# Kernel optimization log

Hardware: AMD Instinct MI355X
Metric: run time of the kernel (lower is better)

The kernel has to match this reference:

```python
import jax, jax.numpy as jnp
import numpy as np

NUM_EXPERTS = 64
TOP_K = 2
CAPACITY_FACTOR = 1.25
D_MODEL = 2048
BATCH, SEQ = 4, 4096


def setup_inputs() -> dict:
    key = jax.random.key(0)
    kx, kw = jax.random.split(key)
    x = jax.random.normal(kx, (BATCH, SEQ, D_MODEL), dtype=jnp.float32)
    # router weight: Linear(input_dim, num_experts, bias=False), init std=0.001
    W = jax.random.normal(kw, (NUM_EXPERTS, D_MODEL), dtype=jnp.float32) * 0.001
    return {"x": x, "W": W}


def reference(x, W):
    B, S, D = x.shape
    N = B * S  # combined batch of tokens
    E = NUM_EXPERTS
    k = TOP_K
    capacity = int(CAPACITY_FACTOR * N * k / E)  # static Python int

    x_flat = x.reshape(N, D)
    router_logits = jnp.einsum('nd,ed->ne', x_flat, W)  # [N, E]
    routing_weights = jax.nn.softmax(router_logits, axis=-1)

    top_k_weights, top_k_indices = jax.lax.top_k(routing_weights, k)  # [N, k]
    top_k_weights = top_k_weights / (top_k_weights.sum(-1, keepdims=True) + 1e-8)

    expert_counts = jnp.zeros((E,), dtype=jnp.float32)
    dispatch_mask = jnp.zeros((N, E), dtype=jnp.float32)
    token_ids = jnp.arange(N)

    # Sequential over k (fixed, small): within a k-step the capacity check uses
    # counts from previous steps only, matching the torch scatter semantics.
    for k_idx in range(k):
        expert_idx = top_k_indices[:, k_idx]            # [N]
        under_cap = expert_counts[expert_idx] < capacity  # [N] bool
        expert_counts = expert_counts + jax.ops.segment_sum(
            under_cap.astype(jnp.float32), expert_idx, num_segments=E)
        # top-k experts are distinct per token, so add == set on zero-init slots
        dispatch_mask = dispatch_mask.at[token_ids, expert_idx].add(
            jnp.where(under_cap, top_k_weights[:, k_idx], 0.0))

    # Tokens that got dropped everywhere go to the least-loaded expert with w=1
    unrouted = dispatch_mask.sum(-1) == 0                     # [N]
    least_loaded = jnp.argmax(capacity - expert_counts)       # scalar
    dispatch_mask = jnp.where(
        unrouted[:, None] & (jnp.arange(E)[None, :] == least_loaded),
        1.0, dispatch_mask)

    normalized_dispatch_mask = dispatch_mask / (dispatch_mask.sum(-1, keepdims=True) + 1e-8)

    router_z_loss = jnp.mean(jnp.square(router_logits))
    counts = normalized_dispatch_mask.sum(0)                  # [E]
    target_count = float(N * k / E)
    load_balance_loss = jnp.mean(jnp.square(counts / float(N) - target_count / float(N)))
    router_loss = 0.001 * jax.lax.stop_gradient(router_z_loss) \
                + 0.001 * jax.lax.stop_gradient(load_balance_loss)

    return (jax.lax.stop_gradient(routing_weights), normalized_dispatch_mask, router_loss)
```

## Files before the change

### kernel.cpp

```cpp
#include <hip/hip_runtime.h>
#include <math.h>

#define N_TOK 16384
#define D_MODEL 2048
#define N_EXP 64
#define CAPACITY 640
#define NREP 8
#define TM 32
#define NSTEP 32

typedef __attribute__((ext_vector_type(8))) _Float16 h8;
typedef __attribute__((ext_vector_type(4))) float f4;

#define AS1 __attribute__((address_space(1)))
#define AS3 __attribute__((address_space(3)))
__device__ __forceinline__ void gld16(const void* g, void* l) {
  __builtin_amdgcn_global_load_lds((const AS1 void*)g, (AS3 void*)l, 16, 0, 0);
}

__global__ __launch_bounds__(256) void k0_cvtw(const float* __restrict__ W,
                                               _Float16* __restrict__ WT) {
  const int lane = threadIdx.x & 63;
  const int c = blockIdx.x * 4 + (threadIdx.x >> 6);
  const int s = c >> 4, q = c & 15;
  const int part = q >> 3, ks = (q >> 2) & 1, nt = q & 3;
  const int e = nt * 16 + (lane & 15);
  const int k = s * 64 + ks * 32 + (lane >> 4) * 8;
  const float* src = W + (size_t)e * D_MODEL + k;
  const float4 a = *(const float4*)src;
  const float4 b = *(const float4*)(src + 4);
  const float f[8] = {a.x, a.y, a.z, a.w, b.x, b.y, b.z, b.w};
  h8 out;
#pragma unroll
  for (int j = 0; j < 8; j++) {
    const float sc = f[j] * 1024.f;
    const _Float16 h = (_Float16)sc;
    out[j] = part ? (_Float16)((sc - (float)h) * 1024.f) : h;
  }
  *(h8*)(WT + (size_t)c * 512 + lane * 8) = out;
}

__global__ __launch_bounds__(256, 2) void k12_gemm_softmax(
    const float* __restrict__ x, const _Float16* __restrict__ WT,
    float* __restrict__ rw_out, int2* __restrict__ top12,
    float2* __restrict__ wts, int* __restrict__ histR,
    float* __restrict__ zR) {
  __shared__ __align__(16) float XS[2][2048];
  __shared__ __align__(16) _Float16 WS[2][8192];
  __shared__ float slog[TM][65];
  __shared__ float zred[4];

  const int t = threadIdx.x;
  const int lane = t & 63;
  const int wid = t >> 6;
  const int m0 = blockIdx.x * TM;
  const int rep = blockIdx.x & (NREP - 1);

  const int i0 = wid * 2;
  const int r0 = i0 * 4 + (lane >> 4);
  const int r1 = r0 + 4;
  const int s16 = lane & 15;
  const float* xs0 = x + (size_t)(m0 + r0) * D_MODEL + ((s16 ^ (r0 & 7)) * 4);
  const float* xs1 = x + (size_t)(m0 + r1) * D_MODEL + ((s16 ^ (r1 & 7)) * 4);
  const _Float16* wsrc = WT + (size_t)(wid * 4) * 512 + lane * 8;

  f4 acc1[2], acc2[2];
#pragma unroll
  for (int i = 0; i < 2; i++) {
    acc1[i] = (f4)(0.f);
    acc2[i] = (f4)(0.f);
  }

#define STAGE(buf, s)                                           \
  {                                                             \
    gld16(xs0 + (s) * 64, &XS[buf][i0 * 256]);                  \
    gld16(xs1 + (s) * 64, &XS[buf][i0 * 256 + 256]);            \
    _Pragma("unroll") for (int j2 = 0; j2 < 4; j2++)            \
        gld16(wsrc + (size_t)(s) * 8192 + j2 * 512,             \
              &WS[buf][(wid * 4 + j2) * 512]);                  \
  }

#define COMPUTE(buf)                                                           \
  {                                                                            \
    _Pragma("unroll") for (int ks = 0; ks < 2; ks++) {                         \
      const h8 bh = *(const h8*)&WS[buf][(ks * 4 + wid) * 512 + lane * 8];     \
      const h8 bl = *(const h8*)&WS[buf][(8 + ks * 4 + wid) * 512 + lane * 8]; \
      _Pragma("unroll") for (int mf = 0; mf < 2; mf++) {                       \
        const int row = mf * 16 + (lane & 15);                                 \
        const int cb = ks * 8 + (lane >> 4) * 2;                               \
        const int sw = lane & 7;                                               \
        const f4 a0 = *(const f4*)&XS[buf][row * 64 + ((cb ^ sw) * 4)];        \
        const f4 a1 = *(const f4*)&XS[buf][row * 64 + (((cb + 1) ^ sw) * 4)];  \
        h8 ah, al;                                                             \
        const float xf[8] = {a0[0], a0[1], a0[2], a0[3],                       \
                             a1[0], a1[1], a1[2], a1[3]};                      \
        _Pragma("unroll") for (int j = 0; j < 8; j++) {                        \
          const _Float16 hv = (_Float16)xf[j];                                 \
          ah[j] = hv;                                                          \
          al[j] = (_Float16)((xf[j] - (float)hv) * 1024.f);                    \
        }                                                                      \
        acc1[mf] = __builtin_amdgcn_mfma_f32_16x16x32_f16(ah, bh, acc1[mf],    \
                                                          0, 0, 0);            \
        acc2[mf] = __builtin_amdgcn_mfma_f32_16x16x32_f16(al, bh, acc2[mf],    \
                                                          0, 0, 0);            \
        acc2[mf] = __builtin_amdgcn_mfma_f32_16x16x32_f16(ah, bl, acc2[mf],    \
                                                          0, 0, 0);            \
      }                                                                        \
    }                                                                          \
  }

  STAGE(0, 0);
  int cur = 0;
  for (int s = 0; s < NSTEP; s++) {
    __syncthreads();
    if (s + 1 < NSTEP) STAGE(cur ^ 1, s + 1);
    COMPUTE(cur);
    cur ^= 1;
  }

  const int cg = lane >> 4, ci = lane & 15;
#pragma unroll
  for (int mf = 0; mf < 2; mf++)
#pragma unroll
    for (int r = 0; r < 4; r++) {
      const float v =
          (acc1[mf][r] + acc2[mf][r] * 0.0009765625f) * 0.0009765625f;
      slog[mf * 16 + cg * 4 + r][wid * 16 + ci] = v;
    }
  __syncthreads();

  float z_acc = 0.f;
  for (int tt = 0; tt < 8; tt++) {
    const int tloc = wid * 8 + tt;
    const int n = m0 + tloc;
    const float v = slog[tloc][lane];
    z_acc += v * v;
    float mx = v;
#pragma unroll
    for (int off = 32; off; off >>= 1) mx = fmaxf(mx, __shfl_xor(mx, off));
    const float p = __expf(v - mx);
    float ssum = p;
#pragma unroll
    for (int off = 32; off; off >>= 1) ssum += __shfl_xor(ssum, off);
    const float rw = p / ssum;
    rw_out[(size_t)n * N_EXP + lane] = rw;

    const unsigned long long b1 = __ballot(v == mx);
    const int i1 = __builtin_ctzll(b1);
    float v2 = (lane == i1) ? -INFINITY : v;
#pragma unroll
    for (int off = 32; off; off >>= 1) v2 = fmaxf(v2, __shfl_xor(v2, off));
    const unsigned long long b2 = __ballot(v == v2) & ~(1ull << i1);
    const int i2 = __builtin_ctzll(b2);
    const float rw1 = __shfl(rw, i1);
    const float rw2 = __shfl(rw, i2);
    if (lane == 0) {
      const float denom = rw1 + rw2 + 1e-8f;
      top12[n] = make_int2(i1, i2);
      wts[n] = make_float2(rw1 / denom, rw2 / denom);
      atomicAdd(&histR[(rep * N_EXP + i1) * 16], 1);
    }
  }
#pragma unroll
  for (int off = 32; off; off >>= 1) z_acc += __shfl_xor(z_acc, off);
  if (lane == 0) zred[wid] = z_acc;
  __syncthreads();
  if (t == 0) atomicAdd(&zR[rep * 16], zred[0] + zred[1] + zred[2] + zred[3]);
}

__global__ __launch_bounds__(256) void k3_dispatch(
    const int2* __restrict__ top12, const float2* __restrict__ wts,
    const int* __restrict__ histR, float* __restrict__ mask_out,
    float* __restrict__ cntR) {
  const int lane = threadIdx.x & 63;
  const int wid = threadIdx.x >> 6;
  const int n = blockIdx.x * 4 + wid;
  const int rep = blockIdx.x & (NREP - 1);

  const int2 ij = top12[n];
  const float2 w = wts[n];
  int h = 0;
#pragma unroll
  for (int r = 0; r < NREP; r++) h += histR[(r * N_EXP + ij.y) * 16];
  const bool allowed = h < CAPACITY;
  const float ssum = w.x + (allowed ? w.y : 0.f);
  const float inv = 1.f / (ssum + 1e-8f);
  float val = 0.f;
  if (lane == ij.x) val = w.x * inv;
  else if (allowed && lane == ij.y) val = w.y * inv;
  mask_out[(size_t)n * N_EXP + lane] = val;
  if (val != 0.f) atomicAdd(&cntR[(rep * N_EXP + lane) * 16], val);
}

__global__ void k4_loss(const float* __restrict__ cntR,
                        const float* __restrict__ zR,
                        float* __restrict__ loss_out) {
  const int lane = threadIdx.x;
  float c = 0.f;
#pragma unroll
  for (int r = 0; r < NREP; r++) c += cntR[(r * N_EXP + lane) * 16];
  const float d = (c - 512.0f) * (1.0f / 16384.0f);
  float v = d * d;
#pragma unroll
  for (int off = 32; off; off >>= 1) v += __shfl_xor(v, off);
  if (lane == 0) {
    float z = 0.f;
#pragma unroll
    for (int r = 0; r < NREP; r++) z += zR[r * 16];
    const float lb = v * (1.0f / 64.0f);
    loss_out[0] = 0.001f * (z * (1.0f / (16384.0f * 64.0f))) + 0.001f * lb;
  }
}

extern "C" void kernel_launch(void* const* d_in, const int* in_sizes, int n_in,
                              void* d_out, int out_size, void* d_ws,
                              size_t ws_size, hipStream_t stream) {
  const float* x = (const float*)d_in[0];
  const float* W = (const float*)d_in[1];
  float* out = (float*)d_out;
  float* rw_out = out;
  float* mask_out = out + (size_t)N_TOK * N_EXP;
  float* loss_out = out + 2 * (size_t)N_TOK * N_EXP;

  char* ws = (char*)d_ws;
  int* histR = (int*)ws;
  float* cntR = (float*)(ws + 32768);
  float* zR = (float*)(ws + 65536);
  int2* top12 = (int2*)(ws + 131072);
  float2* wts = (float2*)(ws + 262144);
  _Float16* WT = (_Float16*)(ws + 393216);

  hipMemsetAsync(histR, 0, 65536 + 512, stream);
  k0_cvtw<<<128, 256, 0, stream>>>(W, WT);
  k12_gemm_softmax<<<512, 256, 0, stream>>>(x, WT, rw_out, top12, wts, histR,
                                            zR);
  k3_dispatch<<<N_TOK / 4, 256, 0, stream>>>(top12, wts, histR, mask_out,
                                             cntR);
  k4_loss<<<1, 64, 0, stream>>>(cntR, zR, loss_out);
}
```

Baseline: 228.9 us.

## Make GEMM warps independent with per-warp triple-buffered LDS pipeline

Restructures the router GEMM so each of two waves owns a 16-token tile across all 64 experts, with its own triple-buffered LDS staging driven by vmcnt waits instead of block-wide barriers. This removes __syncthreads from the k-loop and the cross-wave softmax handoff, and regroups the W fp16 split layout into k-steps of 32. The cost is that every wave now loads the full W slice on its own, so W traffic per token doubles, and blocks shrink to 128 threads.

Result: slower. 234.8 us (+2.6%).

```diff
diff --git a/kernel.cpp b/kernel.cpp
--- a/kernel.cpp
+++ b/kernel.cpp
@@ -6,8 +6,7 @@
 #define N_EXP 64
 #define CAPACITY 640
 #define NREP 8
-#define TM 32
-#define NSTEP 32
+#define NSTEP 64
 
 typedef __attribute__((ext_vector_type(8))) _Float16 h8;
 typedef __attribute__((ext_vector_type(4))) float f4;
@@ -22,10 +21,10 @@
                                                _Float16* __restrict__ WT) {
   const int lane = threadIdx.x & 63;
   const int c = blockIdx.x * 4 + (threadIdx.x >> 6);
-  const int s = c >> 4, q = c & 15;
-  const int part = q >> 3, ks = (q >> 2) & 1, nt = q & 3;
+  const int s = c >> 3, q = c & 7;
+  const int part = q >> 2, nt = q & 3;
   const int e = nt * 16 + (lane & 15);
-  const int k = s * 64 + ks * 32 + (lane >> 4) * 8;
+  const int k = s * 32 + (lane >> 4) * 8;
   const float* src = W + (size_t)e * D_MODEL + k;
   const float4 a = *(const float4*)src;
   const float4 b = *(const float4*)(src + 4);
@@ -40,100 +39,96 @@
   *(h8*)(WT + (size_t)c * 512 + lane * 8) = out;
 }
 
-__global__ __launch_bounds__(256, 2) void k12_gemm_softmax(
+__global__ __launch_bounds__(128, 2) void k12_gemm_softmax(
     const float* __restrict__ x, const _Float16* __restrict__ WT,
     float* __restrict__ rw_out, int2* __restrict__ top12,
     float2* __restrict__ wts, int* __restrict__ histR,
     float* __restrict__ zR) {
-  __shared__ __align__(16) float XS[2][2048];
-  __shared__ __align__(16) _Float16 WS[2][8192];
-  __shared__ float slog[TM][65];
-  __shared__ float zred[4];
+  __shared__ __align__(16) float XR[2][3][512];
+  __shared__ __align__(16) _Float16 WR[2][3][4096];
 
   const int t = threadIdx.x;
   const int lane = t & 63;
-  const int wid = t >> 6;
-  const int m0 = blockIdx.x * TM;
+  const int w = t >> 6;
+  const int m0w = blockIdx.x * 32 + w * 16;
   const int rep = blockIdx.x & (NREP - 1);
 
-  const int i0 = wid * 2;
-  const int r0 = i0 * 4 + (lane >> 4);
-  const int r1 = r0 + 4;
-  const int s16 = lane & 15;
-  const float* xs0 = x + (size_t)(m0 + r0) * D_MODEL + ((s16 ^ (r0 & 7)) * 4);
-  const float* xs1 = x + (size_t)(m0 + r1) * D_MODEL + ((s16 ^ (r1 & 7)) * 4);
-  const _Float16* wsrc = WT + (size_t)(wid * 4) * 512 + lane * 8;
-
-  f4 acc1[2], acc2[2];
-#pragma unroll
-  for (int i = 0; i < 2; i++) {
+  const float* xb = x + (size_t)(m0w + (lane & 15)) * D_MODEL + (lane >> 4) * 8;
+  const _Float16* wb = WT + lane * 8;
+
+  f4 acc1[4], acc2[4];
+#pragma unroll
+  for (int i = 0; i < 4; i++) {
     acc1[i] = (f4)(0.f);
     acc2[i] = (f4)(0.f);
   }
 
-#define STAGE(buf, s)                                           \
-  {                                                             \
-    gld16(xs0 + (s) * 64, &XS[buf][i0 * 256]);                  \
-    gld16(xs1 + (s) * 64, &XS[buf][i0 * 256 + 256]);            \
-    _Pragma("unroll") for (int j2 = 0; j2 < 4; j2++)            \
-        gld16(wsrc + (size_t)(s) * 8192 + j2 * 512,             \
-              &WS[buf][(wid * 4 + j2) * 512]);                  \
-  }
-
-#define COMPUTE(buf)                                                           \
-  {                                                                            \
-    _Pragma("unroll") for (int ks = 0; ks < 2; ks++) {                         \
-      const h8 bh = *(const h8*)&WS[buf][(ks * 4 + wid) * 512 + lane * 8];     \
-      const h8 bl = *(const h8*)&WS[buf][(8 + ks * 4 + wid) * 512 + lane * 8]; \
-      _Pragma("unroll") for (int mf = 0; mf < 2; mf++) {                       \
-        const int row = mf * 16 + (lane & 15);                                 \
-        const int cb = ks * 8 + (lane >> 4) * 2;                               \
-        const int sw = lane & 7;                                               \
-        const f4 a0 = *(const f4*)&XS[buf][row * 64 + ((cb ^ sw) * 4)];        \
-        const f4 a1 = *(const f4*)&XS[buf][row * 64 + (((cb + 1) ^ sw) * 4)];  \
-        h8 ah, al;                                                             \
-        const float xf[8] = {a0[0], a0[1], a0[2], a0[3],                       \
-                             a1[0], a1[1], a1[2], a1[3]};                      \
-        _Pragma("unroll") for (int j = 0; j < 8; j++) {                        \
-          const _Float16 hv = (_Float16)xf[j];                                 \
-          ah[j] = hv;                                                          \
-          al[j] = (_Float16)((xf[j] - (float)hv) * 1024.f);                    \
-        }                                                                      \
-        acc1[mf] = __builtin_amdgcn_mfma_f32_16x16x32_f16(ah, bh, acc1[mf],    \
-                                                          0, 0, 0);            \
-        acc2[mf] = __builtin_amdgcn_mfma_f32_16x16x32_f16(al, bh, acc2[mf],    \
-                                                          0, 0, 0);            \
-        acc2[mf] = __builtin_amdgcn_mfma_f32_16x16x32_f16(ah, bl, acc2[mf],    \
-                                                          0, 0, 0);            \
-      }                                                                        \
-    }                                                                          \
+#define STAGE(slot, s)                                            \
+  {                                                               \
+    gld16(xb + (s) * 32, &XR[w][slot][0]);                        \
+    gld16(xb + (s) * 32 + 4, &XR[w][slot][256]);                  \
+    _Pragma("unroll") for (int c = 0; c < 8; c++)                 \
+        gld16(wb + (size_t)(s) * 4096 + c * 512, &WR[w][slot][c * 512]); \
+  }
+#define WAITV10 asm volatile("s_waitcnt vmcnt(10)" ::: "memory")
+#define WAITV0 asm volatile("s_waitcnt vmcnt(0)" ::: "memory")
+
+#define COMPUTE(slot)                                                       \
+  {                                                                         \
+    const f4 xa0 = *(const f4*)&XR[w][slot][lane * 4];                      \
+    const f4 xa1 = *(const f4*)&XR[w][slot][256 + lane * 4];                \
+    h8 ah, al;                                                              \
+    const float xf[8] = {xa0[0], xa0[1], xa0[2], xa0[3],                    \
+                         xa1[0], xa1[1], xa1[2], xa1[3]};                   \
+    _Pragma("unroll") for (int j = 0; j < 8; j++) {                         \
+      const _Float16 hv = (_Float16)xf[j];                                  \
+      ah[j] = hv;                                                           \
+      al[j] = (_Float16)((xf[j] - (float)hv) * 1024.f);                     \
+    }                                                                       \
+    _Pragma("unroll") for (int nt = 0; nt < 4; nt++) {                      \
+      const h8 bh = *(const h8*)&WR[w][slot][nt * 512 + lane * 8];          \
+      const h8 bl = *(const h8*)&WR[w][slot][(4 + nt) * 512 + lane * 8];    \
+      acc1[nt] = __builtin_amdgcn_mfma_f32_16x16x32_f16(ah, bh, acc1[nt],   \
+                                                        0, 0, 0);           \
+      acc2[nt] = __builtin_amdgcn_mfma_f32_16x16x32_f16(al, bh, acc2[nt],   \
+                                                        0, 0, 0);           \
+      acc2[nt] = __builtin_amdgcn_mfma_f32_16x16x32_f16(ah, bl, acc2[nt],   \
+                                                        0, 0, 0);           \
+    }                                                                       \
   }
 
   STAGE(0, 0);
-  int cur = 0;
-  for (int s = 0; s < NSTEP; s++) {
-    __syncthreads();
-    if (s + 1 < NSTEP) STAGE(cur ^ 1, s + 1);
-    COMPUTE(cur);
-    cur ^= 1;
-  }
-
+  STAGE(1, 1);
+  for (int g = 0; g < 21; g++) {
+    const int s = 3 * g;
+    WAITV10;
+    COMPUTE(0);
+    STAGE(2, s + 2);
+    WAITV10;
+    COMPUTE(1);
+    STAGE(0, s + 3);
+    WAITV10;
+    COMPUTE(2);
+    if (g < 20) STAGE(1, s + 4);
+  }
+  WAITV0;
+  COMPUTE(0);
+
+  float* slog = (float*)&XR[w][0][0];
   const int cg = lane >> 4, ci = lane & 15;
 #pragma unroll
-  for (int mf = 0; mf < 2; mf++)
+  for (int nt = 0; nt < 4; nt++)
 #pragma unroll
     for (int r = 0; r < 4; r++) {
       const float v =
-          (acc1[mf][r] + acc2[mf][r] * 0.0009765625f) * 0.0009765625f;
-      slog[mf * 16 + cg * 4 + r][wid * 16 + ci] = v;
+          (acc1[nt][r] + acc2[nt][r] * 0.0009765625f) * 0.0009765625f;
+      slog[(cg * 4 + r) * 65 + nt * 16 + ci] = v;
     }
-  __syncthreads();
 
   float z_acc = 0.f;
-  for (int tt = 0; tt < 8; tt++) {
-    const int tloc = wid * 8 + tt;
-    const int n = m0 + tloc;
-    const float v = slog[tloc][lane];
+  for (int tt = 0; tt < 16; tt++) {
+    const int n = m0w + tt;
+    const float v = slog[tt * 65 + lane];
     z_acc += v * v;
     float mx = v;
 #pragma unroll
@@ -163,9 +158,7 @@
   }
 #pragma unroll
   for (int off = 32; off; off >>= 1) z_acc += __shfl_xor(z_acc, off);
-  if (lane == 0) zred[wid] = z_acc;
-  __syncthreads();
-  if (t == 0) atomicAdd(&zR[rep * 16], zred[0] + zred[1] + zred[2] + zred[3]);
+  if (lane == 0) atomicAdd(&zR[rep * 16], z_acc);
 }
 
 __global__ __launch_bounds__(256) void k3_dispatch(
@@ -232,7 +225,7 @@
 
   hipMemsetAsync(histR, 0, 65536 + 512, stream);
   k0_cvtw<<<128, 256, 0, stream>>>(W, WT);
-  k12_gemm_softmax<<<512, 256, 0, stream>>>(x, WT, rw_out, top12, wts, histR,
+  k12_gemm_softmax<<<512, 128, 0, stream>>>(x, WT, rw_out, top12, wts, histR,
                                             zR);
   k3_dispatch<<<N_TOK / 4, 256, 0, stream>>>(top12, wts, histR, mask_out,
                                              cntR);
```
